# Optimization experiments

Measured on AMD Instinct MI355X. Metric: run time of the kernel, lower is better.

## Reference

```python
import jax, jax.numpy as jnp
import numpy as np

NUM_HEADS = 16
D_MODEL = 1024


def setup_inputs() -> dict:
    key = jax.random.key(0)
    ks = jax.random.split(key, 12)
    B, S, D = 2, 2048, D_MODEL
    inp = {
        "query": jax.random.normal(ks[0], (B, S, D), dtype=jnp.float32),
        "key": jax.random.normal(ks[1], (B, S, D), dtype=jnp.float32),
        "value": jax.random.normal(ks[2], (B, S, D), dtype=jnp.float32),
        "mask": jax.random.randint(ks[3], (B, 1, S), 0, 2).astype(jnp.bool_),
    }
    # Linear layer params, stored as (in, out) so y = x @ W + b
    sd = 1.0 / np.sqrt(D)
    for i, nm in enumerate(["q", "k", "v", "o"]):
        inp[f"W{nm}"] = jax.random.uniform(ks[4 + 2 * i], (D, D), jnp.float32, -sd, sd)
        inp[f"b{nm}"] = jax.random.uniform(ks[5 + 2 * i], (D,), jnp.float32, -sd, sd)
    return inp


def _split_heads(x):
    # [B, S, D] -> [B, H, S, d_k]
    B, S, D = x.shape
    return x.reshape(B, S, NUM_HEADS, D // NUM_HEADS).transpose(0, 2, 1, 3)


def reference(query, key, value, mask, Wq, bq, Wk, bk, Wv, bv, Wo, bo):
    B, Sq, D = query.shape
    d_k = D // NUM_HEADS
    scale = 1.0 / np.sqrt(d_k)

    q = _split_heads(query @ Wq + bq)   # [B,H,Sq,dk]
    k = _split_heads(key @ Wk + bk)     # [B,H,Sk,dk]
    v = _split_heads(value @ Wv + bv)   # [B,H,Sk,dk]

    scores = jnp.einsum("bhqd,bhkd->bhqk", q, k) * scale  # [B,H,Sq,Sk]
    # mask: [B,1,Sk] bool, True = masked; broadcast over heads and queries
    scores = jnp.where(mask[:, None, :, :], -jnp.inf, scores)
    attn = jax.nn.softmax(scores, axis=-1)
    attn = jnp.nan_to_num(attn, nan=0.0)  # fully-masked rows -> 0 (matches torch)

    ctx = jnp.einsum("bhqk,bhkd->bhqd", attn, v)  # [B,H,Sq,dk]
    ctx = ctx.transpose(0, 2, 1, 3).reshape(B, Sq, D)  # combine heads
    out = ctx @ Wo + bo
    return out
```

## Files before the change

### kernel.cpp

```cpp
#include <hip/hip_runtime.h>


typedef unsigned short u16;
typedef unsigned int u32;
typedef __attribute__((ext_vector_type(8))) short bf16x8;
typedef __attribute__((ext_vector_type(4))) float f32x4;
typedef __attribute__((ext_vector_type(16))) float f32x16;
typedef __attribute__((ext_vector_type(2))) int i32x2;

static __device__ __forceinline__ u16 f2bf(float x) {
  union { float f; u32 i; } v; v.f = x;
  return (u16)((v.i + 0x8000u) >> 16);
}

static __device__ __forceinline__ u32 cvtpk(float lo, float hi) {
  u32 r;
  asm("v_cvt_pk_bf16_f32 %0, %1, %2" : "=v"(r) : "v"(lo), "v"(hi));
  return r;
}

#define MFMA_B16(a, b, c) __builtin_amdgcn_mfma_f32_16x16x32_bf16((a), (b), (c), 0, 0, 0)
#define MFMA32_B16(a, b, c) __builtin_amdgcn_mfma_f32_32x32x16_bf16((a), (b), (c), 0, 0, 0)

__global__ __launch_bounds__(256) void prep_w(
    const float* __restrict__ w0, const float* __restrict__ w1,
    const float* __restrict__ w2, const float* __restrict__ w3,
    u16* __restrict__ t0, u16* __restrict__ t1,
    u16* __restrict__ t2, u16* __restrict__ t3) {
  __shared__ u16 tile[64 * 68];
  const float* W; u16* T;
  switch (blockIdx.z) {
    case 0: W = w0; T = t0; break;
    case 1: W = w1; T = t1; break;
    case 2: W = w2; T = t2; break;
    default: W = w3; T = t3; break;
  }
  const int t = threadIdx.x;
  const int k0 = blockIdx.x * 64, n0 = blockIdx.y * 64;
#pragma unroll
  for (int it = 0; it < 4; ++it) {
    int idx = it * 256 + t;
    int r = idx >> 4, c4 = idx & 15;
    float4 v = *(const float4*)&W[(size_t)(k0 + r) * 1024 + n0 + c4 * 4];
    tile[r * 68 + c4 * 4 + 0] = f2bf(v.x);
    tile[r * 68 + c4 * 4 + 1] = f2bf(v.y);
    tile[r * 68 + c4 * 4 + 2] = f2bf(v.z);
    tile[r * 68 + c4 * 4 + 3] = f2bf(v.w);
  }
  __syncthreads();
#pragma unroll
  for (int it = 0; it < 2; ++it) {
    int idx = it * 256 + t;
    int n = idx >> 3, kc = idx & 7;
    bf16x8 pk;
#pragma unroll
    for (int j = 0; j < 8; ++j) pk[j] = (short)tile[(kc * 8 + j) * 68 + n];
    *(bf16x8*)&T[(size_t)(n0 + n) * 1024 + k0 + kc * 8] = pk;
  }
}

template <int MT, int AMODE, int OMODE>
__global__ __launch_bounds__(256) void gemm_bias(
    const void* a0v, const void* a1v, const void* a2v,
    const u16* __restrict__ Wt,
    const float* b0, const float* b1, const float* b2,
    void* o0, void* o1, void* o2) {
  __shared__ __align__(16) u16 As[MT * 32 * 32];
  __shared__ __align__(16) u16 Bs[128 * 32];
  const int t = threadIdx.x, wave = t >> 6, lane = t & 63;
  const int l15 = lane & 15, quad = lane >> 4;
  const int m0 = blockIdx.x * (MT * 32);
  const int n0 = blockIdx.y * 128;
  const int rg = (OMODE == 3) ? (n0 >> 10) : 0;
  const void* Av = (rg == 0) ? a0v : (rg == 1 ? a1v : a2v);
  const float* bp = (rg == 0) ? b0 : (rg == 1 ? b1 : b2);
  const int nb = (OMODE == 3) ? (n0 & 1023) : n0;
  const int wr = (wave >> 1) * (MT * 16), wc = (wave & 1) * 64;

  const f32x4 fz = {0.f, 0.f, 0.f, 0.f};
  f32x4 acc[MT][4];
#pragma unroll
  for (int mt = 0; mt < MT; ++mt)
#pragma unroll
    for (int nt = 0; nt < 4; ++nt) acc[mt][nt] = fz;

  float4 pa[MT / 2][2]; bf16x8 pab[MT / 2]; bf16x8 pb[2];
#pragma unroll
  for (int s = 0; s < MT / 2; ++s) {
    int idx = s * 256 + t, row = idx >> 2, seg = idx & 3;
    if (AMODE == 1) {
      const float* ap = (const float*)Av + (size_t)(m0 + row) * 1024 + seg * 8;
      pa[s][0] = *(const float4*)ap; pa[s][1] = *(const float4*)(ap + 4);
    } else {
      pab[s] = *(const bf16x8*)((const u16*)Av + (size_t)(m0 + row) * 1024 + seg * 8);
    }
  }
#pragma unroll
  for (int s = 0; s < 2; ++s) {
    int idx = s * 256 + t, row = idx >> 2, seg = idx & 3;
    pb[s] = *(const bf16x8*)&Wt[(size_t)(n0 + row) * 1024 + seg * 8];
  }

  for (int kb = 0; kb < 1024; kb += 32) {
    __syncthreads();
#pragma unroll
    for (int s = 0; s < MT / 2; ++s) {
      int idx = s * 256 + t, row = idx >> 2, seg = idx & 3;
      bf16x8 pk;
      if (AMODE == 1) {
        pk[0] = (short)f2bf(pa[s][0].x); pk[1] = (short)f2bf(pa[s][0].y);
        pk[2] = (short)f2bf(pa[s][0].z); pk[3] = (short)f2bf(pa[s][0].w);
        pk[4] = (short)f2bf(pa[s][1].x); pk[5] = (short)f2bf(pa[s][1].y);
        pk[6] = (short)f2bf(pa[s][1].z); pk[7] = (short)f2bf(pa[s][1].w);
      } else pk = pab[s];
      *(bf16x8*)&As[row * 32 + ((seg ^ ((row >> 1) & 3)) * 8)] = pk;
    }
#pragma unroll
    for (int s = 0; s < 2; ++s) {
      int idx = s * 256 + t, row = idx >> 2, seg = idx & 3;
      *(bf16x8*)&Bs[row * 32 + ((seg ^ ((row >> 1) & 3)) * 8)] = pb[s];
    }
    __syncthreads();
    const int kn = (kb + 32) & 1023;
#pragma unroll
    for (int s = 0; s < MT / 2; ++s) {
      int idx = s * 256 + t, row = idx >> 2, seg = idx & 3;
      if (AMODE == 1) {
        const float* ap = (const float*)Av + (size_t)(m0 + row) * 1024 + kn + seg * 8;
        pa[s][0] = *(const float4*)ap; pa[s][1] = *(const float4*)(ap + 4);
      } else {
        pab[s] = *(const bf16x8*)((const u16*)Av + (size_t)(m0 + row) * 1024 + kn + seg * 8);
      }
    }
#pragma unroll
    for (int s = 0; s < 2; ++s) {
      int idx = s * 256 + t, row = idx >> 2, seg = idx & 3;
      pb[s] = *(const bf16x8*)&Wt[(size_t)(n0 + row) * 1024 + kn + seg * 8];
    }
    bf16x8 a[MT], bfr[4];
#pragma unroll
    for (int mt = 0; mt < MT; ++mt) {
      const int ra = wr + mt * 16 + l15;
      a[mt] = *(const bf16x8*)&As[ra * 32 + ((quad ^ ((ra >> 1) & 3)) * 8)];
    }
#pragma unroll
    for (int nt = 0; nt < 4; ++nt) {
      const int rb = wc + nt * 16 + l15;
      bfr[nt] = *(const bf16x8*)&Bs[rb * 32 + ((quad ^ ((rb >> 1) & 3)) * 8)];
    }
#pragma unroll
    for (int mt = 0; mt < MT; ++mt)
#pragma unroll
      for (int nt = 0; nt < 4; ++nt)
        acc[mt][nt] = MFMA_B16(a[mt], bfr[nt], acc[mt][nt]);
  }

#pragma unroll
  for (int nt = 0; nt < 4; ++nt) {
    const int n = nb + wc + nt * 16 + l15;
    const float bv = bp[n];
#pragma unroll
    for (int mt = 0; mt < MT; ++mt)
#pragma unroll
      for (int r = 0; r < 4; ++r) {
        const int m = m0 + wr + mt * 16 + quad * 4 + r;
        const float val = acc[mt][nt][r] + bv;
        if (OMODE == 2) {
          ((float*)o0)[(size_t)m * 1024 + n] = val;
        } else if (OMODE == 0) {
          ((u16*)o0)[(size_t)m * 1024 + n] = f2bf(val);
        } else {
          if (rg == 0)      ((u16*)o0)[(size_t)m * 1024 + n] = f2bf(val);
          else if (rg == 1) ((u16*)o1)[(size_t)m * 1024 + n] = f2bf(val);
          else {
            const int h = n >> 6, d = n & 63, bb = m >> 11, ss = m & 2047;
            ((u16*)o2)[((size_t)(bb * 16 + h) * 64 + d) * 2048 + ss] = f2bf(val);
          }
        }
      }
  }
}

__global__ __launch_bounds__(256) void attn_fused(
    const u16* Q, const u16* __restrict__ K,
    const u16* __restrict__ Vt, const int* __restrict__ mask,
    u16* ctx) {
  __shared__ __align__(16) u16 Ks[8 * 128 * 8];
  __shared__ __align__(16) u16 Vs[16 * 64 * 8];
  __shared__ __align__(16) float Mf[128];
  const int t = threadIdx.x, wave = t >> 6, lane = t & 63;
  const int l31 = lane & 31, hi = lane >> 5;
  const int lin = blockIdx.y * gridDim.x + blockIdx.x;
  const int xcd = lin & 7, slot = lin >> 3;
  const int bh = xcd + 8 * (slot >> 4);
  const int qt = slot & 15;
  const int b = bh >> 4, h = bh & 15;
  const int q0w = qt * 128 + wave * 32;
  const float cs = 0.125f * 1.44269504f;

  const u16* Qp2 = Q + (size_t)(b * 2048 + q0w) * 1024 + h * 64;
  bf16x8 qb[4];
#pragma unroll
  for (int kd = 0; kd < 4; ++kd)
    qb[kd] = *(const bf16x8*)(Qp2 + (size_t)l31 * 1024 + kd * 16 + hi * 8);

  const u16* Kbase = K + (size_t)(b * 2048) * 1024 + h * 64;
  const u16* Vbase = Vt + (size_t)bh * 64 * 2048;

  bf16x8 gk[4], gv[4];
#pragma unroll
  for (int s = 0; s < 4; ++s) {
    int slot2 = s * 256 + t;
    int kr = slot2 >> 3, ksg = slot2 & 7;
    gk[s] = *(const bf16x8*)&Kbase[(size_t)kr * 1024 + ksg * 8];
    int vr = slot2 >> 4, vsg = slot2 & 15;
    gv[s] = *(const bf16x8*)&Vbase[(size_t)vr * 2048 + vsg * 8];
  }
  int gmv = mask[b * 2048 + (t & 127)];

  bf16x8 onesb;
#pragma unroll
  for (int j = 0; j < 8; ++j) onesb[j] = (short)0x3F80;

  const f32x16 sz = {0.f};
  f32x16 o0a = sz, o1a = sz;
  f32x16 osum = sz;

  for (int kt = 0; kt < 2048; kt += 128) {
    __syncthreads();
#pragma unroll
    for (int s = 0; s < 4; ++s) {
      int slot2 = s * 256 + t;
      int kr = slot2 >> 3, ksg = slot2 & 7;
      *(bf16x8*)&Ks[ksg * 1024 + ((kr ^ (ksg & 7)) * 8)] = gk[s];
      int vr = slot2 >> 4, vsg = slot2 & 15;
      *(bf16x8*)&Vs[vsg * 512 + ((vr ^ (vsg & 7)) * 8)] = gv[s];
    }
    if (t < 128) Mf[t] = gmv ? -__builtin_inff() : 0.f;
    __syncthreads();
    const int kn = (kt + 128) & 2047;
#pragma unroll
    for (int s = 0; s < 4; ++s) {
      int slot2 = s * 256 + t;
      int kr = slot2 >> 3, ksg = slot2 & 7;
      gk[s] = *(const bf16x8*)&Kbase[(size_t)(kn + kr) * 1024 + ksg * 8];
      int vr = slot2 >> 4, vsg = slot2 & 15;
      gv[s] = *(const bf16x8*)&Vbase[(size_t)vr * 2048 + kn + vsg * 8];
    }
    gmv = mask[b * 2048 + kn + (t & 127)];

#pragma unroll
    for (int kg = 0; kg < 4; ++kg) {
      f32x16 S = sz;
#pragma unroll
      for (int kd = 0; kd < 4; ++kd) {
        const int dseg = kd * 2 + hi;
        const bf16x8 kf = *(const bf16x8*)
            &Ks[dseg * 1024 + (((kg * 32 + l31) ^ (dseg & 7)) * 8)];
        S = MFMA32_B16(kf, qb[kd], S);
      }
      u32 W[8];
#pragma unroll
      for (int c = 0; c < 4; ++c) {
        const float4 bias4 = *(const float4*)&Mf[kg * 32 + c * 8 + hi * 4];
        const float p0 = exp2f(fmaf(S[c * 4 + 0], cs, bias4.x));
        const float p1 = exp2f(fmaf(S[c * 4 + 1], cs, bias4.y));
        const float p2 = exp2f(fmaf(S[c * 4 + 2], cs, bias4.z));
        const float p3 = exp2f(fmaf(S[c * 4 + 3], cs, bias4.w));
        W[2 * c + 0] = cvtpk(p0, p1);
        W[2 * c + 1] = cvtpk(p2, p3);
      }
      {
        i32x2 r0 = __builtin_amdgcn_permlane32_swap((int)W[0], (int)W[2], false, false);
        i32x2 r1 = __builtin_amdgcn_permlane32_swap((int)W[1], (int)W[3], false, false);
        i32x2 r2 = __builtin_amdgcn_permlane32_swap((int)W[4], (int)W[6], false, false);
        i32x2 r3 = __builtin_amdgcn_permlane32_swap((int)W[5], (int)W[7], false, false);
        union { bf16x8 v; u32 w[4]; } pa0, pa1;
        pa0.w[0] = (u32)r0[0]; pa0.w[1] = (u32)r1[0];
        pa0.w[2] = (u32)r0[1]; pa0.w[3] = (u32)r1[1];
        pa1.w[0] = (u32)r2[0]; pa1.w[1] = (u32)r3[0];
        pa1.w[2] = (u32)r2[1]; pa1.w[3] = (u32)r3[1];
#pragma unroll
        for (int ks2 = 0; ks2 < 2; ++ks2) {
          const bf16x8 pav = ks2 ? pa1.v : pa0.v;
          const int kseg = (kg * 2 + ks2) * 2 + hi;
          const bf16x8 vf0 = *(const bf16x8*)
              &Vs[kseg * 512 + ((l31 ^ (kseg & 7)) * 8)];
          const bf16x8 vf1 = *(const bf16x8*)
              &Vs[kseg * 512 + (((32 + l31) ^ (kseg & 7)) * 8)];
          o0a = MFMA32_B16(pav, vf0, o0a);
          o1a = MFMA32_B16(pav, vf1, o1a);
          osum = MFMA32_B16(pav, onesb, osum);
        }
      }
    }
  }
  u16* cp = ctx + (size_t)(b * 2048 + q0w) * 1024 + h * 64;
#pragma unroll
  for (int c = 0; c < 4; ++c) {
#pragma unroll
    for (int j = 0; j < 4; ++j) {
      const int e = c * 4 + j;
      const int row = 8 * c + 4 * hi + j;
      const float iv = osum[e] > 0.f ? 1.f / osum[e] : 0.f;
      cp[(size_t)row * 1024 + l31]      = f2bf(o0a[e] * iv);
      cp[(size_t)row * 1024 + 32 + l31] = f2bf(o1a[e] * iv);
    }
  }
}

extern "C" void kernel_launch(void* const* d_in, const int* in_sizes, int n_in,
                              void* d_out, int out_size, void* d_ws, size_t ws_size,
                              hipStream_t stream) {
  const float* q    = (const float*)d_in[0];
  const float* k    = (const float*)d_in[1];
  const float* v    = (const float*)d_in[2];
  const int*   mask = (const int*)d_in[3];
  const float* Wq = (const float*)d_in[4];  const float* bq = (const float*)d_in[5];
  const float* Wk = (const float*)d_in[6];  const float* bk = (const float*)d_in[7];
  const float* Wv = (const float*)d_in[8];  const float* bv = (const float*)d_in[9];
  const float* Wo = (const float*)d_in[10]; const float* bo = (const float*)d_in[11];

  char* ws = (char*)d_ws;
  u16*   Kp  = (u16*)(ws + ((size_t)0 << 20));
  u16*   Vt  = (u16*)(ws + ((size_t)8 << 20));
  float* O32 = (float*)ws;

  char* od = (char*)d_out;
  u16* ctx = (u16*)od;
  u16* WqT = (u16*)(od + ((size_t)8 << 20));
  u16* WkT = (u16*)(od + ((size_t)10 << 20));
  u16* WvT = (u16*)(od + ((size_t)12 << 20));
  u16* WoT = (u16*)(od + ((size_t)14 << 20));

  dim3 blk(256);
  prep_w<<<dim3(16, 16, 4), blk, 0, stream>>>(Wq, Wk, Wv, Wo, WqT, WkT, WvT, WoT);
  gemm_bias<4, 1, 3><<<dim3(32, 24), blk, 0, stream>>>(
      q, k, v, WqT, bq, bk, bv, (void*)ctx, (void*)Kp, (void*)Vt);
  attn_fused<<<dim3(16, 32), dim3(256), 0, stream>>>(ctx, Kp, Vt, mask, ctx);
  gemm_bias<2, 0, 2><<<dim3(64, 8), blk, 0, stream>>>(
      ctx, nullptr, nullptr, WoT, bo, nullptr, nullptr, (void*)O32, nullptr, nullptr);
  hipMemcpyAsync(d_out, O32, (size_t)out_size * sizeof(float),
                 hipMemcpyDeviceToDevice, stream);
}
```

Baseline: 259.0 us.

## Use direct global-to-LDS loads with double buffering in GEMM and attention

Replaces the register-staged global loads followed by LDS stores with global_load_lds DMA transfers into double-buffered shared memory. This applies to the bf16 GEMM paths and to the K/V tiles in the attention kernel. The goal is to drop the register round trip and one barrier per iteration, so loading the next tile overlaps with the MFMA work on the current one. In exchange, LDS use doubles, and correctness now depends on the DMA writes completing before the single barrier. Occupancy may also drop.

```diff
diff --git a/kernel.cpp b/kernel.cpp
--- a/kernel.cpp
+++ b/kernel.cpp
@@ -17,6 +17,12 @@
   u32 r;
   asm("v_cvt_pk_bf16_f32 %0, %1, %2" : "=v"(r) : "v"(lo), "v"(hi));
   return r;
+}
+
+static __device__ __forceinline__ void gload_lds16(const void* g, void* l) {
+  __builtin_amdgcn_global_load_lds(
+      (const __attribute__((address_space(1))) unsigned int*)g,
+      (__attribute__((address_space(3))) unsigned int*)l, 16, 0, 0);
 }
 
 #define MFMA_B16(a, b, c) __builtin_amdgcn_mfma_f32_16x16x32_bf16((a), (b), (c), 0, 0, 0)
@@ -65,8 +71,8 @@
     const u16* __restrict__ Wt,
     const float* b0, const float* b1, const float* b2,
     void* o0, void* o1, void* o2) {
-  __shared__ __align__(16) u16 As[MT * 32 * 32];
-  __shared__ __align__(16) u16 Bs[128 * 32];
+  __shared__ __align__(16) u16 As[(AMODE == 1 ? 1 : 2) * MT * 32 * 32];
+  __shared__ __align__(16) u16 Bs[2 * 128 * 32];
   const int t = threadIdx.x, wave = t >> 6, lane = t & 63;
   const int l15 = lane & 15, quad = lane >> 4;
   const int m0 = blockIdx.x * (MT * 32);
@@ -84,76 +90,90 @@
 #pragma unroll
     for (int nt = 0; nt < 4; ++nt) acc[mt][nt] = fz;
 
-  float4 pa[MT / 2][2]; bf16x8 pab[MT / 2]; bf16x8 pb[2];
-#pragma unroll
-  for (int s = 0; s < MT / 2; ++s) {
-    int idx = s * 256 + t, row = idx >> 2, seg = idx & 3;
-    if (AMODE == 1) {
+  float4 pa[MT / 2][2];
+
+#define STAGE_B(kk, bb)                                                         \
+  {                                                                             \
+    _Pragma("unroll")                                                           \
+    for (int s = 0; s < 2; ++s) {                                               \
+      int idx = s * 256 + t, row = idx >> 2, segp = idx & 3;                    \
+      gload_lds16(&Wt[(size_t)(n0 + row) * 1024 + (kk) +                        \
+                      ((segp ^ ((row >> 1) & 3)) * 8)],                         \
+                  &Bs[(bb) * 4096 + idx * 8]);                                  \
+    }                                                                           \
+  }
+#define STAGE_A_DMA(kk, bb)                                                     \
+  {                                                                             \
+    _Pragma("unroll")                                                           \
+    for (int s = 0; s < MT / 2; ++s) {                                          \
+      int idx = s * 256 + t, row = idx >> 2, segp = idx & 3;                    \
+      gload_lds16((const u16*)Av + (size_t)(m0 + row) * 1024 + (kk) +           \
+                      ((segp ^ ((row >> 1) & 3)) * 8),                          \
+                  &As[(bb) * (MT * 1024) + idx * 8]);                           \
+    }                                                                           \
+  }
+
+  STAGE_B(0, 0);
+  if (AMODE == 1) {
+#pragma unroll
+    for (int s = 0; s < MT / 2; ++s) {
+      int idx = s * 256 + t, row = idx >> 2, seg = idx & 3;
       const float* ap = (const float*)Av + (size_t)(m0 + row) * 1024 + seg * 8;
       pa[s][0] = *(const float4*)ap; pa[s][1] = *(const float4*)(ap + 4);
-    } else {
-      pab[s] = *(const bf16x8*)((const u16*)Av + (size_t)(m0 + row) * 1024 + seg * 8);
-    }
-  }
-#pragma unroll
-  for (int s = 0; s < 2; ++s) {
-    int idx = s * 256 + t, row = idx >> 2, seg = idx & 3;
-    pb[s] = *(const bf16x8*)&Wt[(size_t)(n0 + row) * 1024 + seg * 8];
-  }
-
+    }
+  } else {
+    STAGE_A_DMA(0, 0);
+  }
+
+  int buf = 0;
   for (int kb = 0; kb < 1024; kb += 32) {
     __syncthreads();
-#pragma unroll
-    for (int s = 0; s < MT / 2; ++s) {
-      int idx = s * 256 + t, row = idx >> 2, seg = idx & 3;
-      bf16x8 pk;
-      if (AMODE == 1) {
+    const int kn = (kb + 32) & 1023;
+    if (AMODE == 1) {
+#pragma unroll
+      for (int s = 0; s < MT / 2; ++s) {
+        int idx = s * 256 + t, row = idx >> 2, seg = idx & 3;
+        bf16x8 pk;
         pk[0] = (short)f2bf(pa[s][0].x); pk[1] = (short)f2bf(pa[s][0].y);
         pk[2] = (short)f2bf(pa[s][0].z); pk[3] = (short)f2bf(pa[s][0].w);
         pk[4] = (short)f2bf(pa[s][1].x); pk[5] = (short)f2bf(pa[s][1].y);
         pk[6] = (short)f2bf(pa[s][1].z); pk[7] = (short)f2bf(pa[s][1].w);
-      } else pk = pab[s];
-      *(bf16x8*)&As[row * 32 + ((seg ^ ((row >> 1) & 3)) * 8)] = pk;
-    }
-#pragma unroll
-    for (int s = 0; s < 2; ++s) {
-      int idx = s * 256 + t, row = idx >> 2, seg = idx & 3;
-      *(bf16x8*)&Bs[row * 32 + ((seg ^ ((row >> 1) & 3)) * 8)] = pb[s];
-    }
-    __syncthreads();
-    const int kn = (kb + 32) & 1023;
-#pragma unroll
-    for (int s = 0; s < MT / 2; ++s) {
-      int idx = s * 256 + t, row = idx >> 2, seg = idx & 3;
-      if (AMODE == 1) {
+        *(bf16x8*)&As[row * 32 + ((seg ^ ((row >> 1) & 3)) * 8)] = pk;
+      }
+      __syncthreads();
+      STAGE_B(kn, buf ^ 1);
+#pragma unroll
+      for (int s = 0; s < MT / 2; ++s) {
+        int idx = s * 256 + t, row = idx >> 2, seg = idx & 3;
         const float* ap = (const float*)Av + (size_t)(m0 + row) * 1024 + kn + seg * 8;
         pa[s][0] = *(const float4*)ap; pa[s][1] = *(const float4*)(ap + 4);
-      } else {
-        pab[s] = *(const bf16x8*)((const u16*)Av + (size_t)(m0 + row) * 1024 + kn + seg * 8);
-      }
-    }
-#pragma unroll
-    for (int s = 0; s < 2; ++s) {
-      int idx = s * 256 + t, row = idx >> 2, seg = idx & 3;
-      pb[s] = *(const bf16x8*)&Wt[(size_t)(n0 + row) * 1024 + kn + seg * 8];
+      }
+    } else {
+      STAGE_B(kn, buf ^ 1);
+      STAGE_A_DMA(kn, buf ^ 1);
     }
     bf16x8 a[MT], bfr[4];
 #pragma unroll
     for (int mt = 0; mt < MT; ++mt) {
       const int ra = wr + mt * 16 + l15;
-      a[mt] = *(const bf16x8*)&As[ra * 32 + ((quad ^ ((ra >> 1) & 3)) * 8)];
+      a[mt] = *(const bf16x8*)&As[(AMODE == 0 ? buf * (MT * 1024) : 0) +
+                                  ra * 32 + ((quad ^ ((ra >> 1) & 3)) * 8)];
     }
 #pragma unroll
     for (int nt = 0; nt < 4; ++nt) {
       const int rb = wc + nt * 16 + l15;
-      bfr[nt] = *(const bf16x8*)&Bs[rb * 32 + ((quad ^ ((rb >> 1) & 3)) * 8)];
+      bfr[nt] = *(const bf16x8*)&Bs[buf * 4096 + rb * 32 +
+                                    ((quad ^ ((rb >> 1) & 3)) * 8)];
     }
 #pragma unroll
     for (int mt = 0; mt < MT; ++mt)
 #pragma unroll
       for (int nt = 0; nt < 4; ++nt)
         acc[mt][nt] = MFMA_B16(a[mt], bfr[nt], acc[mt][nt]);
-  }
+    buf ^= 1;
+  }
+#undef STAGE_B
+#undef STAGE_A_DMA
 
 #pragma unroll
   for (int nt = 0; nt < 4; ++nt) {
@@ -185,9 +205,9 @@
     const u16* Q, const u16* __restrict__ K,
     const u16* __restrict__ Vt, const int* __restrict__ mask,
     u16* ctx) {
-  __shared__ __align__(16) u16 Ks[8 * 128 * 8];
-  __shared__ __align__(16) u16 Vs[16 * 64 * 8];
-  __shared__ __align__(16) float Mf[128];
+  __shared__ __align__(16) u16 Ks[2][8192];
+  __shared__ __align__(16) u16 Vs[2][8192];
+  __shared__ __align__(16) float Mf[2][128];
   const int t = threadIdx.x, wave = t >> 6, lane = t & 63;
   const int l31 = lane & 31, hi = lane >> 5;
   const int lin = blockIdx.y * gridDim.x + blockIdx.x;
@@ -207,16 +227,25 @@
   const u16* Kbase = K + (size_t)(b * 2048) * 1024 + h * 64;
   const u16* Vbase = Vt + (size_t)bh * 64 * 2048;
 
-  bf16x8 gk[4], gv[4];
-#pragma unroll
-  for (int s = 0; s < 4; ++s) {
-    int slot2 = s * 256 + t;
-    int kr = slot2 >> 3, ksg = slot2 & 7;
-    gk[s] = *(const bf16x8*)&Kbase[(size_t)kr * 1024 + ksg * 8];
-    int vr = slot2 >> 4, vsg = slot2 & 15;
-    gv[s] = *(const bf16x8*)&Vbase[(size_t)vr * 2048 + vsg * 8];
-  }
+#define STAGE_KV(kt0, bb)                                                       \
+  {                                                                             \
+    _Pragma("unroll")                                                           \
+    for (int s = 0; s < 4; ++s) {                                               \
+      int idx = s * 256 + t;                                                    \
+      int dseg = idx >> 7, key = (idx & 127) ^ (dseg & 7);                      \
+      gload_lds16(&Kbase[(size_t)((kt0) + key) * 1024 + dseg * 8],              \
+                  &Ks[bb][idx * 8]);                                            \
+      int vsg = idx >> 6, d = (idx & 63) ^ (vsg & 7);                           \
+      gload_lds16(&Vbase[(size_t)d * 2048 + (kt0) + vsg * 8],                   \
+                  &Vs[bb][idx * 8]);                                            \
+    }                                                                           \
+  }
+
+  STAGE_KV(0, 0);
   int gmv = mask[b * 2048 + (t & 127)];
+  if (t < 128) Mf[0][t] = gmv ? -__builtin_inff() : 0.f;
+  gmv = mask[b * 2048 + 128 + (t & 127)];
+  __syncthreads();
 
   bf16x8 onesb;
 #pragma unroll
@@ -226,28 +255,12 @@
   f32x16 o0a = sz, o1a = sz;
   f32x16 osum = sz;
 
+  int bufi = 0;
   for (int kt = 0; kt < 2048; kt += 128) {
-    __syncthreads();
-#pragma unroll
-    for (int s = 0; s < 4; ++s) {
-      int slot2 = s * 256 + t;
-      int kr = slot2 >> 3, ksg = slot2 & 7;
-      *(bf16x8*)&Ks[ksg * 1024 + ((kr ^ (ksg & 7)) * 8)] = gk[s];
-      int vr = slot2 >> 4, vsg = slot2 & 15;
-      *(bf16x8*)&Vs[vsg * 512 + ((vr ^ (vsg & 7)) * 8)] = gv[s];
-    }
-    if (t < 128) Mf[t] = gmv ? -__builtin_inff() : 0.f;
-    __syncthreads();
     const int kn = (kt + 128) & 2047;
-#pragma unroll
-    for (int s = 0; s < 4; ++s) {
-      int slot2 = s * 256 + t;
-      int kr = slot2 >> 3, ksg = slot2 & 7;
-      gk[s] = *(const bf16x8*)&Kbase[(size_t)(kn + kr) * 1024 + ksg * 8];
-      int vr = slot2 >> 4, vsg = slot2 & 15;
-      gv[s] = *(const bf16x8*)&Vbase[(size_t)vr * 2048 + kn + vsg * 8];
-    }
-    gmv = mask[b * 2048 + kn + (t & 127)];
+    STAGE_KV(kn, bufi ^ 1);
+    if (t < 128) Mf[bufi ^ 1][t] = gmv ? -__builtin_inff() : 0.f;
+    gmv = mask[b * 2048 + ((kt + 256) & 2047) + (t & 127)];
 
 #pragma unroll
     for (int kg = 0; kg < 4; ++kg) {
@@ -256,13 +269,13 @@
       for (int kd = 0; kd < 4; ++kd) {
         const int dseg = kd * 2 + hi;
         const bf16x8 kf = *(const bf16x8*)
-            &Ks[dseg * 1024 + (((kg * 32 + l31) ^ (dseg & 7)) * 8)];
+            &Ks[bufi][dseg * 1024 + (((kg * 32 + l31) ^ (dseg & 7)) * 8)];
         S = MFMA32_B16(kf, qb[kd], S);
       }
       u32 W[8];
 #pragma unroll
       for (int c = 0; c < 4; ++c) {
-        const float4 bias4 = *(const float4*)&Mf[kg * 32 + c * 8 + hi * 4];
+        const float4 bias4 = *(const float4*)&Mf[bufi][kg * 32 + c * 8 + hi * 4];
         const float p0 = exp2f(fmaf(S[c * 4 + 0], cs, bias4.x));
         const float p1 = exp2f(fmaf(S[c * 4 + 1], cs, bias4.y));
         const float p2 = exp2f(fmaf(S[c * 4 + 2], cs, bias4.z));
@@ -285,16 +298,19 @@
           const bf16x8 pav = ks2 ? pa1.v : pa0.v;
           const int kseg = (kg * 2 + ks2) * 2 + hi;
           const bf16x8 vf0 = *(const bf16x8*)
-              &Vs[kseg * 512 + ((l31 ^ (kseg & 7)) * 8)];
+              &Vs[bufi][kseg * 512 + ((l31 ^ (kseg & 7)) * 8)];
           const bf16x8 vf1 = *(const bf16x8*)
-              &Vs[kseg * 512 + (((32 + l31) ^ (kseg & 7)) * 8)];
+              &Vs[bufi][kseg * 512 + (((32 + l31) ^ (kseg & 7)) * 8)];
           o0a = MFMA32_B16(pav, vf0, o0a);
           o1a = MFMA32_B16(pav, vf1, o1a);
           osum = MFMA32_B16(pav, onesb, osum);
         }
       }
     }
-  }
+    __syncthreads();
+    bufi ^= 1;
+  }
+#undef STAGE_KV
   u16* cp = ctx + (size_t)(b * 2048 + q0w) * 1024 + h * 64;
 #pragma unroll
   for (int c = 0; c < 4; ++c) {
```

After: 272.2 us. 5.1% more time.
